# Kernel tuning notes

Hardware: AMD Instinct MI355X
Metric: run time of the kernel (lower is better)

The kernel has to match this reference:

```python
import jax, jax.numpy as jnp
import numpy as np

BATCH = 4096
DIM = 2048
TEMPERATURE = 0.5


def setup_inputs() -> dict:
    key = jax.random.key(0)
    k1, k2 = jax.random.split(key)
    c_i = jax.random.normal(k1, (BATCH, DIM), dtype=jnp.float32)
    c_j = jax.random.normal(k2, (BATCH, DIM), dtype=jnp.float32)
    return {"c_i": c_i, "c_j": c_j}


def reference(c_i, c_j):
    # Original torch loop computes, for each i,j:
    #   kl[i, j] = sum_k softmax(c_j[j])_k * (log_softmax(c_j[j])_k - log_softmax(c_i[i])_k)
    #   logits = -kl / T ; loss = CE(logits, arange(B), reduction='sum') / B
    # Fused: kl = hneg[None, :] - Li @ Q.T where hneg[j] = sum_k Q[j]*logQ[j].
    B = c_i.shape[0]
    Li = jax.nn.log_softmax(c_i, axis=-1)          # [B, D]
    LQ = jax.nn.log_softmax(c_j, axis=-1)          # [B, D]
    Q = jnp.exp(LQ)                                # softmax(c_j)
    hneg = jnp.sum(Q * LQ, axis=-1)                # [B] negative entropy of each c_j row
    cross = jnp.einsum("id,jd->ij", Li, Q)         # [B, B] sum_k Li[i,k]*Q[j,k]
    kl = hneg[None, :] - cross                     # [B, B]
    logits = -kl / TEMPERATURE
    logp = jax.nn.log_softmax(logits, axis=-1)     # [B, B]
    loss = -jnp.sum(jnp.diagonal(logp)) / B        # CE(sum) / batch_size
    return loss
```

## Files before the change

### kernel.cpp

```cpp
#include <hip/hip_runtime.h>
#include <hip/hip_bf16.h>
#include <math.h>

#define BATCH 4096
#define DIM   2048
#define INV_T 2.0f

#define BM 256
#define BN 256

typedef float floatx4 __attribute__((ext_vector_type(4)));
typedef int   intx4   __attribute__((ext_vector_type(4)));
typedef int   intx8   __attribute__((ext_vector_type(8)));

static __device__ __forceinline__ void gld_lds16(const void* g, void* l) {
  __builtin_amdgcn_global_load_lds(
      (const __attribute__((address_space(1))) void*)g,
      (__attribute__((address_space(3))) void*)l, 16, 0, 0);
}

static __device__ __forceinline__ intx8 comb8(intx4 lo, intx4 hi) {
  intx8 r;
  r[0] = lo[0]; r[1] = lo[1]; r[2] = lo[2]; r[3] = lo[3];
  r[4] = hi[0]; r[5] = hi[1]; r[6] = hi[2]; r[7] = hi[3];
  return r;
}

__global__ __launch_bounds__(256) void prep_kernel(
    const float* __restrict__ ci, const float* __restrict__ cj,
    unsigned char* __restrict__ Li8, unsigned char* __restrict__ Qb8,
    float* __restrict__ hneg, float* __restrict__ isc,
    float* __restrict__ rowsum, float* __restrict__ out)
{
  const int lane = threadIdx.x & 63;
  const int wave = threadIdx.x >> 6;
  const int row = blockIdx.x * 4 + wave;
  const bool isj = row >= BATCH;
  const int r = isj ? row - BATCH : row;
  const float* __restrict__ src = (isj ? cj : ci) + (size_t)r * DIM;

  float v[32];
  #pragma unroll
  for (int i = 0; i < 8; ++i) {
    float4 t = ((const float4*)src)[i * 64 + lane];
    v[i * 4 + 0] = t.x; v[i * 4 + 1] = t.y;
    v[i * 4 + 2] = t.z; v[i * 4 + 3] = t.w;
  }

  float m = v[0];
  #pragma unroll
  for (int i = 1; i < 32; ++i) m = fmaxf(m, v[i]);
  #pragma unroll
  for (int off = 32; off >= 1; off >>= 1) m = fmaxf(m, __shfl_xor(m, off));

  float s = 0.f;
  #pragma unroll
  for (int i = 0; i < 32; ++i) s += __expf(v[i] - m);
  #pragma unroll
  for (int off = 32; off >= 1; off >>= 1) s += __shfl_xor(s, off);
  const float ls = m + __logf(s);

  float scale = 1.f;
  int t = 0;
  if (isj) {
    const float qmax = __expf(m - ls);
    const int be = (int)((__float_as_uint(qmax) >> 23) & 0xff);
    t = 134 - be;
    scale = __uint_as_float((unsigned)(t + 127) << 23);
  }

  unsigned char* dst = (isj ? Qb8 : Li8) + (size_t)r * DIM;
  float h = 0.f;
  #pragma unroll
  for (int i = 0; i < 8; ++i) {
    float f[4];
    #pragma unroll
    for (int j = 0; j < 4; ++j) {
      const float li = v[i * 4 + j] - ls;
      if (isj) {
        const float q = __expf(li);
        h += q * li;
        f[j] = q * scale;
      } else {
        f[j] = li;
      }
    }
    int w = __builtin_amdgcn_cvt_pk_fp8_f32(f[0], f[1], 0, false);
    w = __builtin_amdgcn_cvt_pk_fp8_f32(f[2], f[3], w, true);
    ((int*)dst)[i * 64 + lane] = w;
  }

  if (isj) {
    #pragma unroll
    for (int off = 32; off >= 1; off >>= 1) h += __shfl_xor(h, off);
    if (lane == 0) {
      hneg[r] = h;
      isc[r] = __uint_as_float((unsigned)(127 - t) << 23);
      rowsum[r] = 0.f;
    }
  }
  if (row == 0 && lane == 0) out[0] = 0.f;
}

__global__ __launch_bounds__(512, 1) void gemm_lse_kernel(
    const unsigned char* __restrict__ Li8, const unsigned char* __restrict__ Qb8,
    const float* __restrict__ hneg, const float* __restrict__ isc,
    float* __restrict__ rowsum, float* __restrict__ diag)
{
  __shared__ __attribute__((aligned(16))) unsigned char As_[2][BM * 128];
  __shared__ __attribute__((aligned(16))) unsigned char Bs_[2][BN * 128];

  const int tid  = threadIdx.x;
  const int lin = blockIdx.x;
  const int xc  = lin & 7;
  const int sq  = lin >> 3;
  const int by  = (xc & 3) * 4 + (sq & 3);
  const int bx  = (xc >> 2) * 8 + (sq >> 2);

  const int lane = tid & 63;
  const int wave = tid >> 6;
  const int wm   = wave >> 2;
  const int wn   = wave & 3;

  int soff[4];
  #pragma unroll
  for (int s = 0; s < 4; ++s) {
    const int p = tid + 512 * s;
    const int row = p >> 3;
    const int cbg = (p & 7) ^ (row & 7);
    soff[s] = row * DIM + cbg * 16;
  }
  const unsigned char* Abase = Li8 + (size_t)(by * BM) * DIM;
  const unsigned char* Bbase = Qb8 + (size_t)(bx * BN) * DIM;

  const int rl = lane & 15;
  const int q  = lane >> 4;
  const int sw = rl & 7;

  floatx4 acc[8][4];
  const floatx4 z = {0.f, 0.f, 0.f, 0.f};
  #pragma unroll
  for (int mt = 0; mt < 8; ++mt)
    #pragma unroll
    for (int nt = 0; nt < 4; ++nt) acc[mt][nt] = z;

  #pragma unroll
  for (int s = 0; s < 4; ++s) {
    gld_lds16(Abase + soff[s], &As_[0][0] + (tid + 512 * s) * 16);
    gld_lds16(Bbase + soff[s], &Bs_[0][0] + (tid + 512 * s) * 16);
  }

  for (int t = 0; t < 16; ++t) {
    const unsigned char* Ab = &As_[t & 1][0];
    const unsigned char* Bb = &Bs_[t & 1][0];
    unsigned char* An = &As_[(t & 1) ^ 1][0];
    unsigned char* Bn = &Bs_[(t & 1) ^ 1][0];
    const int kn = (t + 1) * 128;
    const bool pf = (t < 15);

    intx8 bf[4];

    #pragma unroll
    for (int p = 0; p < 4; ++p) {
      if (p == 0) {
        if (pf) {
          gld_lds16(Abase + soff[0] + kn, An + tid * 16);
          gld_lds16(Bbase + soff[0] + kn, Bn + tid * 16);
          asm volatile("s_waitcnt vmcnt(2)" ::: "memory");
        } else {
          asm volatile("s_waitcnt vmcnt(0)" ::: "memory");
        }
        asm volatile("s_barrier" ::: "memory");
        #pragma unroll
        for (int nt = 0; nt < 4; ++nt) {
          const int rb = wn * 64 + nt * 16 + rl;
          const int q0 = rb * 8 + ((2 * q) ^ sw);
          const int q1 = rb * 8 + ((2 * q + 1) ^ sw);
          bf[nt] = comb8(*(const intx4*)(Bb + q0 * 16),
                         *(const intx4*)(Bb + q1 * 16));
        }
      }
      intx8 af0, af1;
      {
        const int ra0 = wm * 128 + (2 * p) * 16 + rl;
        const int a00 = ra0 * 8 + ((2 * q) ^ sw);
        const int a01 = ra0 * 8 + ((2 * q + 1) ^ sw);
        af0 = comb8(*(const intx4*)(Ab + a00 * 16),
                    *(const intx4*)(Ab + a01 * 16));
        const int ra1 = wm * 128 + (2 * p + 1) * 16 + rl;
        const int a10 = ra1 * 8 + ((2 * q) ^ sw);
        const int a11 = ra1 * 8 + ((2 * q + 1) ^ sw);
        af1 = comb8(*(const intx4*)(Ab + a10 * 16),
                    *(const intx4*)(Ab + a11 * 16));
      }
      if (p != 0) {
        if (pf) {
          gld_lds16(Abase + soff[p] + kn, An + (tid + 512 * p) * 16);
          gld_lds16(Bbase + soff[p] + kn, Bn + (tid + 512 * p) * 16);
        }
        asm volatile("s_barrier" ::: "memory");
      }
      __builtin_amdgcn_s_setprio(1);
      #pragma unroll
      for (int nt = 0; nt < 4; ++nt)
        acc[2 * p + 0][nt] = __builtin_amdgcn_mfma_scale_f32_16x16x128_f8f6f4(
            af0, bf[nt], acc[2 * p + 0][nt],
            0, 0,
            0, 127,
            0, 127);
      #pragma unroll
      for (int nt = 0; nt < 4; ++nt)
        acc[2 * p + 1][nt] = __builtin_amdgcn_mfma_scale_f32_16x16x128_f8f6f4(
            af1, bf[nt], acc[2 * p + 1][nt],
            0, 0, 0, 127, 0, 127);
      __builtin_amdgcn_s_setprio(0);
      asm volatile("s_barrier" ::: "memory");
    }
  }

  const int col0 = bx * BN + wn * 64 + rl;
  float hn[4], sc[4];
  #pragma unroll
  for (int nt = 0; nt < 4; ++nt) {
    hn[nt] = hneg[col0 + nt * 16];
    sc[nt] = isc[col0 + nt * 16];
  }
  const int row0 = by * BM + wm * 128 + (q << 2);

  if (bx == by && wm == (wn >> 1) && q == (rl >> 2)) {
    #pragma unroll
    for (int half = 0; half < 2; ++half) {
      #pragma unroll
      for (int nt = 0; nt < 4; ++nt) {
        #pragma unroll
        for (int rr = 0; rr < 4; ++rr) {
          if ((wn & 1) == half && (rl & 3) == rr)
            diag[bx * BN + wn * 64 + nt * 16 + rl] =
                acc[half * 4 + nt][nt][rr] * sc[nt];
        }
      }
    }
  }

  #pragma unroll
  for (int mt = 0; mt < 8; ++mt) {
    #pragma unroll
    for (int rr = 0; rr < 4; ++rr) {
      float p = 0.f;
      #pragma unroll
      for (int nt = 0; nt < 4; ++nt)
        p += __expf(INV_T * (acc[mt][nt][rr] * sc[nt] - hn[nt]));
      p += __shfl_xor(p, 1);
      p += __shfl_xor(p, 2);
      p += __shfl_xor(p, 4);
      p += __shfl_xor(p, 8);
      if (rl == 0)
        atomicAdd(&rowsum[row0 + mt * 16 + rr], p);
    }
  }
}

__global__ __launch_bounds__(256) void finalize_kernel(
    const float* __restrict__ hneg, const float* __restrict__ rowsum,
    const float* __restrict__ diag, float* __restrict__ out)
{
  const int i = blockIdx.x * 256 + threadIdx.x;
  const int lane = threadIdx.x & 63;
  const int wave = threadIdx.x >> 6;

  float c = __logf(rowsum[i]) - INV_T * (diag[i] - hneg[i]);
  #pragma unroll
  for (int off = 32; off >= 1; off >>= 1) c += __shfl_xor(c, off);

  __shared__ float red[4];
  if (lane == 0) red[wave] = c;
  __syncthreads();
  if (threadIdx.x == 0)
    atomicAdd(out, (red[0] + red[1] + red[2] + red[3]) * (1.0f / BATCH));
}

extern "C" void kernel_launch(void* const* d_in, const int* in_sizes, int n_in,
                              void* d_out, int out_size, void* d_ws, size_t ws_size,
                              hipStream_t stream) {
  const float* ci = (const float*)d_in[0];
  const float* cj = (const float*)d_in[1];
  float* out = (float*)d_out;

  unsigned char* Li8 = (unsigned char*)d_ws;
  unsigned char* Qb8 = Li8 + (size_t)BATCH * DIM;
  float* hneg   = (float*)(Qb8 + (size_t)BATCH * DIM);
  float* isc    = hneg + BATCH;
  float* rowsum = isc + BATCH;
  float* diag   = rowsum + BATCH;

  prep_kernel<<<2 * BATCH / 4, 256, 0, stream>>>(ci, cj, Li8, Qb8, hneg, isc, rowsum, out);
  gemm_lse_kernel<<<(BATCH / BM) * (BATCH / BN), 512, 0, stream>>>(Li8, Qb8, hneg, isc, rowsum, diag);
  finalize_kernel<<<BATCH / 256, 256, 0, stream>>>(hneg, rowsum, diag, out);
}
```

Baseline: 144.6 us.

## Issue whole next-tile prefetch upfront and cut per-phase barriers in GEMM loop

Restructures the K-loop of the fp8 MFMA GEMM. Each iteration now issues all eight global-to-LDS prefetches for the next tile at the start, waits only for the previous tile, and synchronises with one barrier before and one after compute. The old schedule spread the prefetches across four phases with a barrier in every phase. The A fragments are now double-buffered in registers so each LDS read overlaps the previous MFMA group. This is meant to cut barrier stalls and improve overlap, at the cost of a burstier load issue pattern and different register pressure.

Result: no change. 142.8 us (-1.3%).

```diff
diff --git a/kernel.cpp b/kernel.cpp
--- a/kernel.cpp
+++ b/kernel.cpp
@@ -151,71 +151,63 @@
   }
 
   for (int t = 0; t < 16; ++t) {
-    const unsigned char* Ab = &As_[t & 1][0];
-    const unsigned char* Bb = &Bs_[t & 1][0];
-    unsigned char* An = &As_[(t & 1) ^ 1][0];
-    unsigned char* Bn = &Bs_[(t & 1) ^ 1][0];
+    const int cur = t & 1;
+    const unsigned char* Ab = &As_[cur][0];
+    const unsigned char* Bb = &Bs_[cur][0];
+    unsigned char* An = &As_[cur ^ 1][0];
+    unsigned char* Bn = &Bs_[cur ^ 1][0];
     const int kn = (t + 1) * 128;
-    const bool pf = (t < 15);
+
+    if (t < 15) {
+      #pragma unroll
+      for (int s = 0; s < 4; ++s) {
+        gld_lds16(Abase + soff[s] + kn, An + (tid + 512 * s) * 16);
+        gld_lds16(Bbase + soff[s] + kn, Bn + (tid + 512 * s) * 16);
+      }
+      asm volatile("s_waitcnt vmcnt(8)" ::: "memory");
+    } else {
+      asm volatile("s_waitcnt vmcnt(0)" ::: "memory");
+    }
+    asm volatile("s_barrier" ::: "memory");
 
     intx8 bf[4];
-
-    #pragma unroll
-    for (int p = 0; p < 4; ++p) {
-      if (p == 0) {
-        if (pf) {
-          gld_lds16(Abase + soff[0] + kn, An + tid * 16);
-          gld_lds16(Bbase + soff[0] + kn, Bn + tid * 16);
-          asm volatile("s_waitcnt vmcnt(2)" ::: "memory");
-        } else {
-          asm volatile("s_waitcnt vmcnt(0)" ::: "memory");
-        }
-        asm volatile("s_barrier" ::: "memory");
-        #pragma unroll
-        for (int nt = 0; nt < 4; ++nt) {
-          const int rb = wn * 64 + nt * 16 + rl;
-          const int q0 = rb * 8 + ((2 * q) ^ sw);
-          const int q1 = rb * 8 + ((2 * q + 1) ^ sw);
-          bf[nt] = comb8(*(const intx4*)(Bb + q0 * 16),
-                         *(const intx4*)(Bb + q1 * 16));
-        }
-      }
-      intx8 af0, af1;
-      {
-        const int ra0 = wm * 128 + (2 * p) * 16 + rl;
-        const int a00 = ra0 * 8 + ((2 * q) ^ sw);
-        const int a01 = ra0 * 8 + ((2 * q + 1) ^ sw);
-        af0 = comb8(*(const intx4*)(Ab + a00 * 16),
-                    *(const intx4*)(Ab + a01 * 16));
-        const int ra1 = wm * 128 + (2 * p + 1) * 16 + rl;
-        const int a10 = ra1 * 8 + ((2 * q) ^ sw);
-        const int a11 = ra1 * 8 + ((2 * q + 1) ^ sw);
-        af1 = comb8(*(const intx4*)(Ab + a10 * 16),
-                    *(const intx4*)(Ab + a11 * 16));
-      }
-      if (p != 0) {
-        if (pf) {
-          gld_lds16(Abase + soff[p] + kn, An + (tid + 512 * p) * 16);
-          gld_lds16(Bbase + soff[p] + kn, Bn + (tid + 512 * p) * 16);
-        }
-        asm volatile("s_barrier" ::: "memory");
+    #pragma unroll
+    for (int nt = 0; nt < 4; ++nt) {
+      const int rb = wn * 64 + nt * 16 + rl;
+      const int q0 = rb * 8 + ((2 * q) ^ sw);
+      const int q1 = rb * 8 + ((2 * q + 1) ^ sw);
+      bf[nt] = comb8(*(const intx4*)(Bb + q0 * 16),
+                     *(const intx4*)(Bb + q1 * 16));
+    }
+    intx8 af[2];
+    {
+      const int ra = wm * 128 + rl;
+      const int a0 = ra * 8 + ((2 * q) ^ sw);
+      const int a1 = ra * 8 + ((2 * q + 1) ^ sw);
+      af[0] = comb8(*(const intx4*)(Ab + a0 * 16),
+                    *(const intx4*)(Ab + a1 * 16));
+    }
+    #pragma unroll
+    for (int s = 0; s < 8; ++s) {
+      if (s < 7) {
+        const int ra = wm * 128 + (s + 1) * 16 + rl;
+        const int a0 = ra * 8 + ((2 * q) ^ sw);
+        const int a1 = ra * 8 + ((2 * q + 1) ^ sw);
+        af[(s + 1) & 1] = comb8(*(const intx4*)(Ab + a0 * 16),
+                                *(const intx4*)(Ab + a1 * 16));
       }
       __builtin_amdgcn_s_setprio(1);
       #pragma unroll
       for (int nt = 0; nt < 4; ++nt)
-        acc[2 * p + 0][nt] = __builtin_amdgcn_mfma_scale_f32_16x16x128_f8f6f4(
-            af0, bf[nt], acc[2 * p + 0][nt],
+        acc[s][nt] = __builtin_amdgcn_mfma_scale_f32_16x16x128_f8f6f4(
+            af[s & 1], bf[nt], acc[s][nt],
             0, 0,
             0, 127,
             0, 127);
-      #pragma unroll
-      for (int nt = 0; nt < 4; ++nt)
-        acc[2 * p + 1][nt] = __builtin_amdgcn_mfma_scale_f32_16x16x128_f8f6f4(
-            af1, bf[nt], acc[2 * p + 1][nt],
-            0, 0, 0, 127, 0, 127);
       __builtin_amdgcn_s_setprio(0);
-      asm volatile("s_barrier" ::: "memory");
-    }
+    }
+
+    asm volatile("s_barrier" ::: "memory");
   }
 
   const int col0 = bx * BN + wn * 64 + rl;
```
